# Kernel tuning notes

Measured on AMD Instinct MI355X. Metric: run time of the kernel, lower is better.

## Reference

```python
import jax, jax.numpy as jnp
import numpy as np

NB_KNN = (10, 20, 100, 200)   # values of k to evaluate; max_k = 200
T = 0.07                       # softmax temperature
NUM_CLASSES = 1000


def setup_inputs() -> dict:
    key = jax.random.key(0)
    k1, k2, k3 = jax.random.split(key, 3)
    features_rank = jax.random.normal(k1, (256, 512), jnp.float32)      # (B, d) query features
    train_features = jax.random.normal(k2, (100000, 512), jnp.float32)  # (N, d) train bank
    train_labels = jax.random.randint(k3, (100000,), 0, NUM_CLASSES)     # (N,) int labels
    return {"features_rank": features_rank, "train_features": train_features,
            "train_labels": train_labels}


def _knn_probs(features_rank, train_features, train_labels):
    max_k = max(NB_KNN)
    # similarity: (B, N) = (B, d) @ (d, N)  -- mirrors torch.mm(broadcasted, train_features_rank_T)
    sims = features_rank @ train_features.T
    topk_sims, idx = jax.lax.top_k(sims, max_k)          # (B, max_k), sorted descending
    neighbors = train_labels[idx]                         # (B, max_k) gathered labels
    w = jax.nn.softmax(topk_sims / T, axis=1)             # (B, max_k) neighbor weights
    B = features_rank.shape[0]
    rows = jnp.arange(B)[:, None]                         # (B, 1) row indices for scatter
    # Instead of materializing one_hot (B, max_k, C) and summing prefixes,
    # scatter-add the first k weights into per-class buckets (same math, fused).
    probs = [jnp.zeros((B, NUM_CLASSES), w.dtype).at[rows, neighbors[:, :k]].add(w[:, :k])
             for k in NB_KNN]
    return jnp.stack(probs, axis=0)                       # (len(NB_KNN), B, C)


def reference(features_rank, train_features, train_labels):
    return _knn_probs(features_rank, train_features, train_labels)
```

## Files before the change

### kernel.cpp

```cpp
#include <hip/hip_runtime.h>
#include <math.h>

#define KDIM   512
#define NCLS   1000
#define CUTOFF 3.0f
#define MAXCAP 4096
#define BN     64
#define BK     64
#define NSTAGE (KDIM / BK)

typedef __attribute__((ext_vector_type(8))) short  short8;
typedef __attribute__((ext_vector_type(4))) float  floatx4;

__device__ __forceinline__ unsigned enc_f(float f) {
    unsigned u = __float_as_uint(f);
    return (u & 0x80000000u) ? ~u : (u | 0x80000000u);
}
__device__ __forceinline__ float dec_f(unsigned k) {
    unsigned u = (k & 0x80000000u) ? (k & 0x7FFFFFFFu) : ~k;
    return __uint_as_float(u);
}
__device__ __forceinline__ unsigned short f2bf(float f) {
    unsigned u = __float_as_uint(f);
    u += 0x7FFFu + ((u >> 16) & 1u);
    return (unsigned short)(u >> 16);
}
__device__ __forceinline__ float bf2f(unsigned short h) {
    return __uint_as_float(((unsigned)h) << 16);
}

__global__ void k_prep(const float* __restrict__ A, unsigned short* __restrict__ af,
                       unsigned* __restrict__ cnt, unsigned* __restrict__ gmax, int Brows) {
    int t = blockIdx.x * blockDim.x + threadIdx.x;
    if (t < Brows) { cnt[t] = 0u; gmax[t] = enc_f(-3.0e38f); }
    if (t >= Brows * (KDIM / 8)) return;
    int r = t >> 6;
    int o = t & 63;
    int s16 = r >> 4, c = o >> 2, kq = o & 3;
    int lane = kq * 16 + (r & 15);
    const float* src = A + (size_t)r * KDIM + o * 8;
    size_t bhi = ((size_t)((s16 * 16 + c) * 2 + 0) * 64 + lane) * 8;
    size_t blo = ((size_t)((s16 * 16 + c) * 2 + 1) * 64 + lane) * 8;
#pragma unroll
    for (int j = 0; j < 8; ++j) {
        float f = src[j];
        unsigned short h = f2bf(f);
        af[bhi + j] = h;
        af[blo + j] = f2bf(f - bf2f(h));
    }
}

__global__ __launch_bounds__(512, 4) void k_gemm(
    const float* __restrict__ Bt,
    const unsigned short* __restrict__ af,
    float* __restrict__ cand_val, int* __restrict__ cand_idx,
    unsigned* __restrict__ cnt, unsigned* __restrict__ gmax,
    int N, int cap)
{
    __shared__ short8 BsH[2][512];
    __shared__ short8 BsL[2][512];

    const int tid  = threadIdx.x;
    const int lane = tid & 63;
    const int wid  = tid >> 6;
    const int colBase = blockIdx.x * BN;

    const int nl  = tid >> 3;
    const int k8  = (tid & 7) * 8;
    const int gcol = colBase + nl;
    const bool colok = (gcol < N);
    const float* bsrc = Bt + (size_t)gcol * KDIM + k8;
    const int chw = k8 >> 5;
    const int kqw = (k8 >> 3) & 3;
    const int ctw = (nl >> 4) & 3;
    const int fidw = chw * 4 + ctw;
    const int lfw  = kqw * 16 + (nl & 15);
    const int slotw = fidw * 64 + (lfw ^ (kqw * 2 + chw));

    floatx4 acc[2][4];
#pragma unroll
    for (int rt = 0; rt < 2; ++rt)
#pragma unroll
        for (int ct = 0; ct < 4; ++ct)
            acc[rt][ct] = (floatx4){0.f, 0.f, 0.f, 0.f};

    const float4 z4 = make_float4(0.f, 0.f, 0.f, 0.f);
    float4 c0 = colok ? *(const float4*)(bsrc)          : z4;
    float4 c1 = colok ? *(const float4*)(bsrc + 4)      : z4;
    float4 n0 = colok ? *(const float4*)(bsrc + BK)     : z4;
    float4 n1 = colok ? *(const float4*)(bsrc + BK + 4) : z4;

    {
        union { float4 v[2]; float f[8]; } P;
        union { short8 v; unsigned short u[8]; } H, L;
        P.v[0] = c0; P.v[1] = c1;
#pragma unroll
        for (int j = 0; j < 8; ++j) {
            unsigned short h = f2bf(P.f[j]);
            H.u[j] = h; L.u[j] = f2bf(P.f[j] - bf2f(h));
        }
        BsH[0][slotw] = H.v; BsL[0][slotw] = L.v;
    }
    __syncthreads();

    for (int s = 0; s < NSTAGE; ++s) {
        if (s + 1 < NSTAGE) {
            c0 = n0; c1 = n1;
            if (s + 2 < NSTAGE) {
                const float* p = bsrc + (s + 2) * BK;
                n0 = colok ? *(const float4*)(p)     : z4;
                n1 = colok ? *(const float4*)(p + 4) : z4;
            }
            union { float4 v[2]; float f[8]; } P;
            union { short8 v; unsigned short u[8]; } H, L;
            P.v[0] = c0; P.v[1] = c1;
#pragma unroll
            for (int j = 0; j < 8; ++j) {
                unsigned short h = f2bf(P.f[j]);
                H.u[j] = h; L.u[j] = f2bf(P.f[j] - bf2f(h));
            }
            BsH[(s + 1) & 1][slotw] = H.v; BsL[(s + 1) & 1][slotw] = L.v;
        }

#pragma unroll
        for (int chunk = 0; chunk < 2; ++chunk) {
            const int cg = s * 2 + chunk;
            short8 aH[2], aL[2];
#pragma unroll
            for (int rt = 0; rt < 2; ++rt) {
                const int s16 = wid * 2 + rt;
                size_t sl = (size_t)((s16 * 16 + cg) * 2) * 64 + lane;
                aH[rt] = *(const short8*)(af + sl * 8);
                aL[rt] = *(const short8*)(af + (sl + 64) * 8);
            }
            const int g = (lane >> 4) * 2 + chunk;
#pragma unroll
            for (int ct = 0; ct < 4; ++ct) {
                const int idx = (chunk * 4 + ct) * 64 + (lane ^ g);
                short8 bh = BsH[s & 1][idx];
                short8 bl = BsL[s & 1][idx];
#pragma unroll
                for (int rt = 0; rt < 2; ++rt) {
                    acc[rt][ct] = __builtin_amdgcn_mfma_f32_16x16x32_bf16(aH[rt], bh, acc[rt][ct], 0, 0, 0);
                    acc[rt][ct] = __builtin_amdgcn_mfma_f32_16x16x32_bf16(aH[rt], bl, acc[rt][ct], 0, 0, 0);
                    acc[rt][ct] = __builtin_amdgcn_mfma_f32_16x16x32_bf16(aL[rt], bh, acc[rt][ct], 0, 0, 0);
                }
            }
        }
        __syncthreads();
    }

    const int q   = lane >> 4;
    const int n15 = lane & 15;
#pragma unroll
    for (int rt = 0; rt < 2; ++rt) {
#pragma unroll
        for (int reg = 0; reg < 4; ++reg) {
            const int row = wid * 32 + rt * 16 + q * 4 + reg;
            float m = fmaxf(fmaxf(acc[rt][0][reg], acc[rt][1][reg]),
                            fmaxf(acc[rt][2][reg], acc[rt][3][reg]));
#pragma unroll
            for (int off = 1; off < 16; off <<= 1) m = fmaxf(m, __shfl_xor(m, off));
            unsigned oldk = 0u;
            if (n15 == 0) oldk = atomicMax(&gmax[row], enc_f(m));
            oldk = (unsigned)__shfl((int)oldk, lane & 48);
            const float thr = fmaxf(dec_f(oldk), m) - CUTOFF;
#pragma unroll
            for (int ct = 0; ct < 4; ++ct) {
                const float v = acc[rt][ct][reg];
                const int col = colBase + ct * 16 + n15;
                if (v >= thr && col < N) {
                    unsigned p = atomicAdd(&cnt[row], 1u);
                    if (p < (unsigned)cap) {
                        cand_val[(size_t)row * cap + p] = v;
                        cand_idx[(size_t)row * cap + p] = col;
                    }
                }
            }
        }
    }
}

__global__ __launch_bounds__(256) void k_finalize(
    const float* __restrict__ cand_val,
    const int* __restrict__ cand_idx,
    const unsigned* __restrict__ cnt,
    const unsigned* __restrict__ gmax,
    const int* __restrict__ labels,
    float* __restrict__ out,
    int Brows, int cap)
{
    __shared__ float s_val[256];
    __shared__ int   s_idx[256];
    __shared__ int   s_n;
    const int row = blockIdx.x;
    const int tid = threadIdx.x;
    if (tid == 0) s_n = 0;
    __syncthreads();

    const float m   = dec_f(gmax[row]);
    const float thr = m - CUTOFF;
    const int n = min((int)cnt[row], cap);
    for (int i = tid; i < n; i += 256) {
        float v = cand_val[(size_t)row * cap + i];
        if (v >= thr) {
            int p = atomicAdd(&s_n, 1);
            if (p < 256) { s_val[p] = v; s_idx[p] = cand_idx[(size_t)row * cap + i]; }
        }
    }
    __syncthreads();

    for (int c = tid; c < 4 * NCLS; c += 256) {
        int s = c / NCLS, cc = c - s * NCLS;
        out[(size_t)s * ((size_t)Brows * NCLS) + (size_t)row * NCLS + cc] = 0.f;
    }
    __syncthreads();

    if (tid == 0) {
        int ns = min(s_n, 256);
        for (int i = 1; i < ns; ++i) {
            float v = s_val[i]; int ix = s_idx[i];
            int j = i - 1;
            while (j >= 0 && s_val[j] < v) { s_val[j+1] = s_val[j]; s_idx[j+1] = s_idx[j]; --j; }
            s_val[j+1] = v; s_idx[j+1] = ix;
        }
        if (ns > 200) ns = 200;
        float Z = 0.f;
        for (int i = 0; i < ns; ++i) Z += expf((s_val[i] - m) / 0.07f);
        float invZ = 1.f / Z;
        const int kv[4] = {10, 20, 100, 200};
        for (int i = 0; i < ns; ++i) {
            float w = expf((s_val[i] - m) / 0.07f) * invZ;
            int lab = labels[s_idx[i]];
#pragma unroll
            for (int s = 0; s < 4; ++s)
                if (i < kv[s])
                    out[(size_t)s * ((size_t)Brows * NCLS) + (size_t)row * NCLS + lab] += w;
        }
    }
}

extern "C" void kernel_launch(void* const* d_in, const int* in_sizes, int n_in,
                              void* d_out, int out_size, void* d_ws, size_t ws_size,
                              hipStream_t stream) {
    const float* A      = (const float*)d_in[0];
    const float* Bt     = (const float*)d_in[1];
    const int*   labels = (const int*)d_in[2];
    float* out = (float*)d_out;

    const int Brows = in_sizes[0] / KDIM;
    const int N     = in_sizes[2];

    size_t af_elems = (size_t)Brows * KDIM * 2;
    unsigned short* af = (unsigned short*)d_ws;
    unsigned* cnt  = (unsigned*)(af + af_elems);
    unsigned* gmax = cnt + Brows;
    char* rest = (char*)(gmax + Brows);
    size_t used  = (size_t)(rest - (char*)d_ws);
    size_t avail = (ws_size > used) ? (ws_size - used) : 0;
    int cap = (int)((avail / ((size_t)Brows * 8)) < (size_t)MAXCAP
                        ? (avail / ((size_t)Brows * 8)) : (size_t)MAXCAP);
    if (cap < 1) cap = 1;
    float* cand_val = (float*)rest;
    int*   cand_idx = (int*)(cand_val + (size_t)Brows * cap);

    k_prep<<<(Brows * (KDIM / 8) + 255) / 256, 256, 0, stream>>>(A, af, cnt, gmax, Brows);
    k_gemm<<<(N + BN - 1) / BN, 512, 0, stream>>>(Bt, af, cand_val, cand_idx, cnt, gmax, N, cap);
    k_finalize<<<Brows, 256, 0, stream>>>(cand_val, cand_idx, cnt, gmax, labels, out, Brows, cap);
}
```

Measured before the change: 395.1 us.

## Halve GEMM block threads with 4 row tiles per wave; parallelize finalize ranking

The GEMM block drops from 512 to 256 threads. Each wave now covers 64 query rows (four 16-row tiles) instead of 32, and each thread converts 16 B elements instead of 8, which raises register use and per-wave MFMA reuse of the shared B tile. The finalize kernel replaces the single-thread insertion sort and serial scatter with a parallel rank-by-counting scheme, a block reduction for the softmax denominator, and shared-memory atomic accumulation that is written out once. The candidate buffer grows to 512 entries. The risks are lower GEMM occupancy from the larger accumulator, and O(n^2) comparisons in the rank computation.

New measurement: 412.2 us. +4.3%, slower.

```diff
diff --git a/kernel.cpp b/kernel.cpp
--- a/kernel.cpp
+++ b/kernel.cpp
@@ -8,6 +8,7 @@
 #define BN     64
 #define BK     64
 #define NSTAGE (KDIM / BK)
+#define FCAP   512
 
 typedef __attribute__((ext_vector_type(8))) short  short8;
 typedef __attribute__((ext_vector_type(4))) float  floatx4;
@@ -50,7 +51,7 @@
     }
 }
 
-__global__ __launch_bounds__(512, 4) void k_gemm(
+__global__ __launch_bounds__(256, 3) void k_gemm(
     const float* __restrict__ Bt,
     const unsigned short* __restrict__ af,
     float* __restrict__ cand_val, int* __restrict__ cand_idx,
@@ -65,70 +66,81 @@
     const int wid  = tid >> 6;
     const int colBase = blockIdx.x * BN;
 
-    const int nl  = tid >> 3;
-    const int k8  = (tid & 7) * 8;
+    const int nl   = tid >> 2;
+    const int kseg = (tid & 3) * 16;
     const int gcol = colBase + nl;
     const bool colok = (gcol < N);
-    const float* bsrc = Bt + (size_t)gcol * KDIM + k8;
-    const int chw = k8 >> 5;
-    const int kqw = (k8 >> 3) & 3;
-    const int ctw = (nl >> 4) & 3;
-    const int fidw = chw * 4 + ctw;
-    const int lfw  = kqw * 16 + (nl & 15);
-    const int slotw = fidw * 64 + (lfw ^ (kqw * 2 + chw));
-
-    floatx4 acc[2][4];
-#pragma unroll
-    for (int rt = 0; rt < 2; ++rt)
+    const float* bsrc = Bt + (size_t)gcol * KDIM + kseg;
+
+    int slotw[2];
+#pragma unroll
+    for (int oo = 0; oo < 2; ++oo) {
+        const int k8  = kseg + oo * 8;
+        const int chw = k8 >> 5;
+        const int kqw = (k8 >> 3) & 3;
+        const int ctw = (nl >> 4) & 3;
+        const int fidw = chw * 4 + ctw;
+        const int lfw  = kqw * 16 + (nl & 15);
+        slotw[oo] = fidw * 64 + (lfw ^ (kqw * 2 + chw));
+    }
+
+    floatx4 acc[4][4];
+#pragma unroll
+    for (int rt = 0; rt < 4; ++rt)
 #pragma unroll
         for (int ct = 0; ct < 4; ++ct)
             acc[rt][ct] = (floatx4){0.f, 0.f, 0.f, 0.f};
 
     const float4 z4 = make_float4(0.f, 0.f, 0.f, 0.f);
-    float4 c0 = colok ? *(const float4*)(bsrc)          : z4;
-    float4 c1 = colok ? *(const float4*)(bsrc + 4)      : z4;
-    float4 n0 = colok ? *(const float4*)(bsrc + BK)     : z4;
-    float4 n1 = colok ? *(const float4*)(bsrc + BK + 4) : z4;
-
-    {
-        union { float4 v[2]; float f[8]; } P;
-        union { short8 v; unsigned short u[8]; } H, L;
-        P.v[0] = c0; P.v[1] = c1;
-#pragma unroll
-        for (int j = 0; j < 8; ++j) {
-            unsigned short h = f2bf(P.f[j]);
-            H.u[j] = h; L.u[j] = f2bf(P.f[j] - bf2f(h));
-        }
-        BsH[0][slotw] = H.v; BsL[0][slotw] = L.v;
-    }
+    float4 c0 = colok ? *(const float4*)(bsrc)           : z4;
+    float4 c1 = colok ? *(const float4*)(bsrc + 4)       : z4;
+    float4 c2 = colok ? *(const float4*)(bsrc + 8)       : z4;
+    float4 c3 = colok ? *(const float4*)(bsrc + 12)      : z4;
+    float4 n0 = colok ? *(const float4*)(bsrc + BK)      : z4;
+    float4 n1 = colok ? *(const float4*)(bsrc + BK + 4)  : z4;
+    float4 n2 = colok ? *(const float4*)(bsrc + BK + 8)  : z4;
+    float4 n3 = colok ? *(const float4*)(bsrc + BK + 12) : z4;
+
+    auto cvw = [&](int buf, float4 a0, float4 a1, float4 a2, float4 a3) {
+        union { float4 v[4]; float f[16]; } P;
+        P.v[0] = a0; P.v[1] = a1; P.v[2] = a2; P.v[3] = a3;
+#pragma unroll
+        for (int oo = 0; oo < 2; ++oo) {
+            union { short8 v; unsigned short u[8]; } H, L;
+#pragma unroll
+            for (int j = 0; j < 8; ++j) {
+                float f = P.f[oo * 8 + j];
+                unsigned short h = f2bf(f);
+                H.u[j] = h; L.u[j] = f2bf(f - bf2f(h));
+            }
+            BsH[buf][slotw[oo]] = H.v;
+            BsL[buf][slotw[oo]] = L.v;
+        }
+    };
+
+    cvw(0, c0, c1, c2, c3);
     __syncthreads();
 
     for (int s = 0; s < NSTAGE; ++s) {
         if (s + 1 < NSTAGE) {
-            c0 = n0; c1 = n1;
+            c0 = n0; c1 = n1; c2 = n2; c3 = n3;
             if (s + 2 < NSTAGE) {
                 const float* p = bsrc + (s + 2) * BK;
-                n0 = colok ? *(const float4*)(p)     : z4;
-                n1 = colok ? *(const float4*)(p + 4) : z4;
-            }
-            union { float4 v[2]; float f[8]; } P;
-            union { short8 v; unsigned short u[8]; } H, L;
-            P.v[0] = c0; P.v[1] = c1;
-#pragma unroll
-            for (int j = 0; j < 8; ++j) {
-                unsigned short h = f2bf(P.f[j]);
-                H.u[j] = h; L.u[j] = f2bf(P.f[j] - bf2f(h));
-            }
-            BsH[(s + 1) & 1][slotw] = H.v; BsL[(s + 1) & 1][slotw] = L.v;
+                n0 = colok ? *(const float4*)(p)      : z4;
+                n1 = colok ? *(const float4*)(p + 4)  : z4;
+                n2 = colok ? *(const float4*)(p + 8)  : z4;
+                n3 = colok ? *(const float4*)(p + 12) : z4;
+            }
+            cvw((s + 1) & 1, c0, c1, c2, c3);
         }
 
 #pragma unroll
         for (int chunk = 0; chunk < 2; ++chunk) {
             const int cg = s * 2 + chunk;
-            short8 aH[2], aL[2];
-#pragma unroll
-            for (int rt = 0; rt < 2; ++rt) {
-                const int s16 = wid * 2 + rt;
+            short8 aH[4], aL[4];
+#pragma unroll
+            for (int rt = 0; rt < 4; ++rt) {
+                const int s16 = wid * 4 + rt;
                 size_t sl = (size_t)((s16 * 16 + cg) * 2) * 64 + lane;
                 aH[rt] = *(const short8*)(af + sl * 8);
                 aL[rt] = *(const short8*)(af + (sl + 64) * 8);
@@ -140,7 +152,7 @@
                 short8 bh = BsH[s & 1][idx];
                 short8 bl = BsL[s & 1][idx];
 #pragma unroll
-                for (int rt = 0; rt < 2; ++rt) {
+                for (int rt = 0; rt < 4; ++rt) {
                     acc[rt][ct] = __builtin_amdgcn_mfma_f32_16x16x32_bf16(aH[rt], bh, acc[rt][ct], 0, 0, 0);
                     acc[rt][ct] = __builtin_amdgcn_mfma_f32_16x16x32_bf16(aH[rt], bl, acc[rt][ct], 0, 0, 0);
                     acc[rt][ct] = __builtin_amdgcn_mfma_f32_16x16x32_bf16(aL[rt], bh, acc[rt][ct], 0, 0, 0);
@@ -153,10 +165,10 @@
     const int q   = lane >> 4;
     const int n15 = lane & 15;
 #pragma unroll
-    for (int rt = 0; rt < 2; ++rt) {
+    for (int rt = 0; rt < 4; ++rt) {
 #pragma unroll
         for (int reg = 0; reg < 4; ++reg) {
-            const int row = wid * 32 + rt * 16 + q * 4 + reg;
+            const int row = wid * 64 + rt * 16 + q * 4 + reg;
             float m = fmaxf(fmaxf(acc[rt][0][reg], acc[rt][1][reg]),
                             fmaxf(acc[rt][2][reg], acc[rt][3][reg]));
 #pragma unroll
@@ -190,9 +202,13 @@
     float* __restrict__ out,
     int Brows, int cap)
 {
-    __shared__ float s_val[256];
-    __shared__ int   s_idx[256];
+    __shared__ float s_val[FCAP];
+    __shared__ int   s_idx[FCAP];
+    __shared__ float s_out[4 * NCLS];
     __shared__ int   s_n;
+    __shared__ float s_part[4];
+    __shared__ float s_Z;
+
     const int row = blockIdx.x;
     const int tid = threadIdx.x;
     if (tid == 0) s_n = 0;
@@ -205,38 +221,66 @@
         float v = cand_val[(size_t)row * cap + i];
         if (v >= thr) {
             int p = atomicAdd(&s_n, 1);
-            if (p < 256) { s_val[p] = v; s_idx[p] = cand_idx[(size_t)row * cap + i]; }
-        }
+            if (p < FCAP) { s_val[p] = v; s_idx[p] = cand_idx[(size_t)row * cap + i]; }
+        }
+    }
+    for (int c = tid; c < 4 * NCLS; c += 256) s_out[c] = 0.f;
+    __syncthreads();
+    const int ns = min(s_n, FCAP);
+
+    float e0 = 0.f, e1 = 0.f;
+    int   r0 = 0x7fffffff, r1 = 0x7fffffff;
+    int   lab0 = 0, lab1 = 0;
+    if (tid < ns) {
+        const float v = s_val[tid]; const int ix = s_idx[tid];
+        int rk = 0;
+        for (int j = 0; j < ns; ++j) {
+            const float vj = s_val[j];
+            rk += (vj > v || (vj == v && s_idx[j] < ix)) ? 1 : 0;
+        }
+        r0 = rk;
+        if (rk < 200) { e0 = expf((v - m) * (1.0f / 0.07f)); lab0 = labels[ix]; }
+    }
+    if (tid + 256 < ns) {
+        const int i2 = tid + 256;
+        const float v = s_val[i2]; const int ix = s_idx[i2];
+        int rk = 0;
+        for (int j = 0; j < ns; ++j) {
+            const float vj = s_val[j];
+            rk += (vj > v || (vj == v && s_idx[j] < ix)) ? 1 : 0;
+        }
+        r1 = rk;
+        if (rk < 200) { e1 = expf((v - m) * (1.0f / 0.07f)); lab1 = labels[ix]; }
+    }
+
+    float part = e0 + e1;
+#pragma unroll
+    for (int off = 32; off >= 1; off >>= 1) part += __shfl_down(part, off);
+    if ((tid & 63) == 0) s_part[tid >> 6] = part;
+    __syncthreads();
+    if (tid == 0) s_Z = (s_part[0] + s_part[1]) + (s_part[2] + s_part[3]);
+    __syncthreads();
+    const float invZ = 1.0f / s_Z;
+
+    if (r0 < 200) {
+        const float w = e0 * invZ;
+        if (r0 < 10)  atomicAdd(&s_out[0 * NCLS + lab0], w);
+        if (r0 < 20)  atomicAdd(&s_out[1 * NCLS + lab0], w);
+        if (r0 < 100) atomicAdd(&s_out[2 * NCLS + lab0], w);
+        atomicAdd(&s_out[3 * NCLS + lab0], w);
+    }
+    if (r1 < 200) {
+        const float w = e1 * invZ;
+        if (r1 < 10)  atomicAdd(&s_out[0 * NCLS + lab1], w);
+        if (r1 < 20)  atomicAdd(&s_out[1 * NCLS + lab1], w);
+        if (r1 < 100) atomicAdd(&s_out[2 * NCLS + lab1], w);
+        atomicAdd(&s_out[3 * NCLS + lab1], w);
     }
     __syncthreads();
 
     for (int c = tid; c < 4 * NCLS; c += 256) {
-        int s = c / NCLS, cc = c - s * NCLS;
-        out[(size_t)s * ((size_t)Brows * NCLS) + (size_t)row * NCLS + cc] = 0.f;
-    }
-    __syncthreads();
-
-    if (tid == 0) {
-        int ns = min(s_n, 256);
-        for (int i = 1; i < ns; ++i) {
-            float v = s_val[i]; int ix = s_idx[i];
-            int j = i - 1;
-            while (j >= 0 && s_val[j] < v) { s_val[j+1] = s_val[j]; s_idx[j+1] = s_idx[j]; --j; }
-            s_val[j+1] = v; s_idx[j+1] = ix;
-        }
-        if (ns > 200) ns = 200;
-        float Z = 0.f;
-        for (int i = 0; i < ns; ++i) Z += expf((s_val[i] - m) / 0.07f);
-        float invZ = 1.f / Z;
-        const int kv[4] = {10, 20, 100, 200};
-        for (int i = 0; i < ns; ++i) {
-            float w = expf((s_val[i] - m) / 0.07f) * invZ;
-            int lab = labels[s_idx[i]];
-#pragma unroll
-            for (int s = 0; s < 4; ++s)
-                if (i < kv[s])
-                    out[(size_t)s * ((size_t)Brows * NCLS) + (size_t)row * NCLS + lab] += w;
-        }
+        const int sl = c / NCLS, cc = c - sl * NCLS;
+        out[(size_t)sl * ((size_t)Brows * NCLS) + (size_t)row * NCLS + cc] = s_out[c];
     }
 }
 
@@ -265,6 +309,6 @@
     int*   cand_idx = (int*)(cand_val + (size_t)Brows * cap);
 
     k_prep<<<(Brows * (KDIM / 8) + 255) / 256, 256, 0, stream>>>(A, af, cnt, gmax, Brows);
-    k_gemm<<<(N + BN - 1) / BN, 512, 0, stream>>>(Bt, af, cand_val, cand_idx, cnt, gmax, N, cap);
+    k_gemm<<<(N + BN - 1) / BN, 256, 0, stream>>>(Bt, af, cand_val, cand_idx, cnt, gmax, N, cap);
     k_finalize<<<Brows, 256, 0, stream>>>(cand_val, cand_idx, cnt, gmax, labels, out, Brows, cap);
 }
```
